# Optimization experiments

Measured on AMD Instinct MI355X. Metric: run time of the kernel, lower is better.

## Reference

```python
import jax, jax.numpy as jnp
import numpy as np

N_IN, D_IN, N_OUT, D_OUT = 1152, 8, 10, 16
ROUTINGS, NUM_BG = 3, 1
C, H, W = 1, 28, 28
BATCH = 128
DEC_IN = N_OUT * D_OUT  # 160, projection_type=None -> dec_feature_size = outcaps_size


def squash(x, axis=-1):
    norm = jnp.linalg.norm(x, axis=axis, keepdims=True)
    scale = norm ** 2 / (1.0 + norm ** 2) / (norm + 1e-8)
    return scale * x


def scale_coef(x, num_bg):
    # x: [B, n_out] or [B, n_out, n_in]; min/max normalize over dim 1,
    # excluding the last num_bg (background) capsules, then floor at 0.5.
    if num_bg > 0:
        xm = x[:, : x.shape[1] - num_bg]
    else:
        xm = x
    mn = jnp.min(xm, axis=1, keepdims=True)
    mx = jnp.max(xm, axis=1, keepdims=True)
    out = (xm - mn) / jnp.maximum(mx - mn, 1e-6)  # vrange (0,1)
    if num_bg > 0:
        out = jnp.concatenate([out, jnp.zeros_like(out[:, :num_bg])], axis=1)
    return jnp.maximum(out, 0.5)


def decode(capsflat, W1, b1, W2, b2, W3, b3):
    # fcn decoder (eval mode: dropout is identity): 160 -> 512 -> 1024 -> C*H*W
    h = jax.nn.relu(capsflat @ W1 + b1)
    h = jax.nn.relu(h @ W2 + b2)
    return jax.nn.sigmoid(h @ W3 + b3)


def setup_inputs() -> dict:
    key = jax.random.key(0)
    ks = jax.random.split(key, 9)
    return {
        'incaps': jax.random.normal(ks[0], (BATCH, N_IN, D_IN), jnp.float32),
        'x_input': jax.random.uniform(ks[1], (BATCH, C, H, W), jnp.float32),
        'weight': 0.1 * jax.random.normal(ks[2], (N_OUT, N_IN, D_OUT, D_IN), jnp.float32),
        'W1': 0.05 * jax.random.normal(ks[3], (DEC_IN, 512), jnp.float32),
        'b1': jnp.zeros((512,), jnp.float32),
        'W2': 0.05 * jax.random.normal(ks[4], (512, 1024), jnp.float32),
        'b2': jnp.zeros((1024,), jnp.float32),
        'W3': 0.05 * jax.random.normal(ks[5], (1024, C * H * W), jnp.float32),
        'b3': jnp.zeros((C * H * W,), jnp.float32),
    }


def reference(incaps, x_input, weight, W1, b1, W2, b2, W3, b3):
    B = incaps.shape[0]
    # outcaps_hat: matmul(weight, incaps[:,None,:,:,None]).squeeze(-1)
    hat = jnp.einsum('nkoi,bki->bnko', weight, incaps)  # [B, n_out, n_in, d_out]
    hat_d = jax.lax.stop_gradient(hat)
    rc = jnp.ones((B, N_OUT, N_IN), hat.dtype)
    eye = jnp.eye(N_OUT, dtype=hat.dtype)
    x_flat = x_input.reshape(B, 1, -1)
    for _ in range(ROUTINGS - 1):
        # squash over capsule dim, weighted sum over input capsules
        outcaps = squash(jnp.sum(rc[..., None] * hat_d, axis=2, keepdims=True))  # [B,n,1,d]
        b = jnp.sum(outcaps * hat_d, axis=-1)  # agreement [B, n_out, n_in]
        c = scale_coef(b, NUM_BG)
        objcaps = outcaps[:, :, 0, :]  # [B, n_out, d_out]
        # get_every_obj_rscore vectorized: mask one object capsule at a time
        masked = objcaps[:, None, :, :] * eye[None, :, :, None]  # [B, n_obj, n_out, d]
        recon = decode(masked.reshape(B, N_OUT, DEC_IN), W1, b1, W2, b2, W3, b3)  # [B,n_obj,CHW]
        rscore = -jnp.sum((x_flat - recon) ** 2, axis=-1)  # neg MSE-sum, [B, n_obj]
        r = scale_coef(rscore, NUM_BG)
        rc = c * r[:, :, None]
    # final iteration uses non-detached hat
    outcaps = squash(jnp.sum(rc[..., None] * hat, axis=2, keepdims=True))
    return outcaps[:, :, 0, :]  # [B, n_out, d_out]
```

## Files before the change

### kernel.cpp

```cpp
#include <hip/hip_runtime.h>
#include <math.h>

#define BATCH  128
#define NIN    1152
#define DIN    8
#define NOUTC  10
#define DOUT   16
#define H1DIM  512
#define H2DIM  1024
#define PIX    784
#define NROWS  (BATCH * NOUTC)
#define GN     32
#define PARTS  25
#define PSTR   32

typedef __attribute__((ext_vector_type(8))) __bf16 bf16x8;
typedef __attribute__((ext_vector_type(4))) float  f32x4;
typedef __attribute__((ext_vector_type(4))) unsigned int u32x4;

__device__ __forceinline__ float bf2f(unsigned int u) {
    union { unsigned int i; float f; } v; v.i = u << 16; return v.f;
}
__device__ __forceinline__ ushort f2bf(float f) {
    union { float f; unsigned int i; } v; v.f = f;
    unsigned int r = v.i + 0x7FFFu + ((v.i >> 16) & 1u);
    return (ushort)(r >> 16);
}
__device__ __forceinline__ float ldin(const void* p, size_t i, int isbf) {
    return isbf ? bf2f(((const ushort*)p)[i]) : ((const float*)p)[i];
}
__device__ __forceinline__ bf16x8 frag_of(uint4 u) {
    return __builtin_bit_cast(bf16x8, u);
}
__device__ __forceinline__ bf16x8 ld_frag(const ushort* p) {
    return frag_of(*(const uint4*)p);
}
__device__ __forceinline__ void unpack8(uint4 u, float* f) {
    f[0] = bf2f(u.x & 0xffffu); f[1] = bf2f(u.x >> 16);
    f[2] = bf2f(u.y & 0xffffu); f[3] = bf2f(u.y >> 16);
    f[4] = bf2f(u.z & 0xffffu); f[5] = bf2f(u.z >> 16);
    f[6] = bf2f(u.w & 0xffffu); f[7] = bf2f(u.w >> 16);
}

__device__ __forceinline__ int detect_bf(const void* w, int* cntS) {
    int tid = threadIdx.x, nt = blockDim.x;
    if (tid == 0) *cntS = 0;
    __syncthreads();
    const ushort* u = (const ushort*)w;
    int c = 0;
    for (int s = tid; s < 512; s += nt) {
        int e = (u[s * 2] >> 7) & 0xFF;
        if (e >= 88 && e <= 140) c++;
    }
    atomicAdd(cntS, c);
    __syncthreads();
    return (*cntS >= 384) ? 1 : 0;
}

struct PrepArgs {
    const void* w;
    const void* src[7];
    ushort*     dst[7];
    int         n[7];
    int*        flag;
};

__global__ __launch_bounds__(256) void prep_kernel(PrepArgs a)
{
    __shared__ int cntS;
    __shared__ ushort tile[32][33];
    int tid = threadIdx.x;
    int isbf = detect_bf(a.w, &cntS);
    int seg = blockIdx.y;
    if (seg == 0 && blockIdx.x == 0 && tid == 0) *a.flag = isbf;

    if (seg <= 4) {
        int n = a.n[seg];
        int stride = gridDim.x * 256;
        ushort* d = a.dst[seg];
        if (isbf) {
            const ushort* s = (const ushort*)a.src[seg];
            for (int i = blockIdx.x * 256 + tid; i < n; i += stride) d[i] = s[i];
        } else {
            const float* s = (const float*)a.src[seg];
            for (int i = blockIdx.x * 256 + tid; i < n; i += stride) d[i] = f2bf(s[i]);
        }
        return;
    }
    int R = (seg == 5) ? H1DIM : H2DIM;
    int C = (seg == 5) ? H2DIM : PIX;
    int tilesX = (seg == 5) ? 32 : 25;
    int tilesY = (seg == 5) ? 16 : 32;
    int t = blockIdx.x;
    if (t >= tilesX * tilesY) return;
    int tx2 = t % tilesX, ty2 = t / tilesX;
    int c0 = tx2 * 32, r0 = ty2 * 32;
    const void* in = a.src[seg];
    ushort* out = a.dst[seg];
    int tx = tid & 31, ty = tid >> 5;
    for (int i = ty; i < 32; i += 8) {
        int r = r0 + i, c = c0 + tx;
        tile[i][tx] = (r < R && c < C) ? f2bf(ldin(in, (size_t)r * C + c, isbf)) : (ushort)0;
    }
    __syncthreads();
    for (int i = ty; i < 32; i += 8) {
        int c = c0 + i, r = r0 + tx;
        if (c < C && r < R) out[(size_t)c * R + r] = tile[tx][i];
    }
}

__global__ __launch_bounds__(256) void hat_prep_kernel(
    const void* __restrict__ inc,
    PrepArgs a,
    ushort* __restrict__ hatG)
{
    __shared__ int cntS;
    __shared__ ushort tile[32][33];
    int tid = threadIdx.x;
    int isbf = detect_bf(a.w, &cntS);

    if (blockIdx.z >= NOUTC) {
        int p = (blockIdx.z - NOUTC) * 144 + blockIdx.y * 9 + blockIdx.x;
        if (p == 0 && tid == 0) *a.flag = isbf;
        if (p < 528) {
            for (int t = p; t < 1312; t += 528) {
                int seg = (t < 512) ? 5 : 6;
                int tt  = (seg == 5) ? t : t - 512;
                int R = (seg == 5) ? H1DIM : H2DIM;
                int C = (seg == 5) ? H2DIM : PIX;
                int tilesX = (seg == 5) ? 32 : 25;
                int tx2 = tt % tilesX, ty2 = tt / tilesX;
                int c0 = tx2 * 32, r0 = ty2 * 32;
                const void* in = a.src[seg];
                ushort* out = a.dst[seg];
                int tx = tid & 31, ty = tid >> 5;
                for (int i = ty; i < 32; i += 8) {
                    int r = r0 + i, c = c0 + tx;
                    tile[i][tx] = (r < R && c < C) ? f2bf(ldin(in, (size_t)r * C + c, isbf)) : (ushort)0;
                }
                __syncthreads();
                for (int i = ty; i < 32; i += 8) {
                    int c = c0 + i, r = r0 + tx;
                    if (c < C && r < R) out[(size_t)c * R + r] = tile[tx][i];
                }
                __syncthreads();
            }
        } else {
            int base = (p - 528) * 256 + tid;
            const int stride = 48 * 256;
            #pragma unroll
            for (int seg = 0; seg <= 4; seg++) {
                int n = a.n[seg];
                ushort* d = a.dst[seg];
                if (isbf) {
                    const ushort* s = (const ushort*)a.src[seg];
                    for (int i = base; i < n; i += stride) d[i] = s[i];
                } else {
                    const float* s = (const float*)a.src[seg];
                    for (int i = base; i < n; i += stride) d[i] = f2bf(s[i]);
                }
            }
        }
        return;
    }

    int kc = blockIdx.x, bc = blockIdx.y, n = blockIdx.z;
    int k  = kc * 128 + (tid >> 1);
    int oh = (tid & 1) << 3;
    int b0 = bc * 8;

    size_t wbase = ((size_t)n * NIN + k) * DOUT + oh;

    if (isbf) {
        uint4 wr[8], ir[8];
        const uint4* wp = (const uint4*)((const ushort*)a.w + wbase * DIN);
        const ushort* ip = (const ushort*)inc;
        #pragma unroll
        for (int j = 0; j < 8; j++) wr[j] = wp[j];
        #pragma unroll
        for (int bl = 0; bl < 8; bl++)
            ir[bl] = *(const uint4*)(ip + ((size_t)(b0 + bl) * NIN + k) * DIN);
        float wf[8][8];
        #pragma unroll
        for (int j = 0; j < 8; j++) unpack8(wr[j], wf[j]);
        #pragma unroll
        for (int bl = 0; bl < 8; bl++) {
            float xi[8];
            unpack8(ir[bl], xi);
            unsigned int hh[8];
            #pragma unroll
            for (int j = 0; j < 8; j++) {
                float s = wf[j][0] * xi[0] + wf[j][1] * xi[1] + wf[j][2] * xi[2] +
                          wf[j][3] * xi[3] + wf[j][4] * xi[4] + wf[j][5] * xi[5] +
                          wf[j][6] * xi[6] + wf[j][7] * xi[7];
                hh[j] = f2bf(s);
            }
            u32x4 ov = { hh[0] | (hh[1] << 16), hh[2] | (hh[3] << 16),
                         hh[4] | (hh[5] << 16), hh[6] | (hh[7] << 16) };
            *(u32x4*)(hatG + (((size_t)((b0 + bl) * NOUTC + n) * NIN + k) * DOUT + oh)) = ov;
        }
    } else {
        float4 wlo[8], whi[8], ilo[8], ihi[8];
        const float4* wp = (const float4*)((const float*)a.w + wbase * DIN);
        const float*  ip = (const float*)inc;
        #pragma unroll
        for (int j = 0; j < 8; j++) { wlo[j] = wp[2 * j]; whi[j] = wp[2 * j + 1]; }
        #pragma unroll
        for (int bl = 0; bl < 8; bl++) {
            const float4* q = (const float4*)(ip + ((size_t)(b0 + bl) * NIN + k) * DIN);
            ilo[bl] = q[0]; ihi[bl] = q[1];
        }
        #pragma unroll
        for (int bl = 0; bl < 8; bl++) {
            float4 lo = ilo[bl], hi = ihi[bl];
            unsigned int hh[8];
            #pragma unroll
            for (int j = 0; j < 8; j++) {
                float s = wlo[j].x * lo.x + wlo[j].y * lo.y + wlo[j].z * lo.z +
                          wlo[j].w * lo.w + whi[j].x * hi.x + whi[j].y * hi.y +
                          whi[j].z * hi.z + whi[j].w * hi.w;
                hh[j] = f2bf(s);
            }
            u32x4 ov = { hh[0] | (hh[1] << 16), hh[2] | (hh[3] << 16),
                         hh[4] | (hh[5] << 16), hh[6] | (hh[7] << 16) };
            *(u32x4*)(hatG + (((size_t)((b0 + bl) * NOUTC + n) * NIN + k) * DOUT + oh)) = ov;
        }
    }
}

__global__ __launch_bounds__(512, 4) void reduce_hat512(
    const ushort* __restrict__ hatG,
    const ushort* __restrict__ bsPrev,
    const float*  __restrict__ partials,
    int iter0,
    const ushort* __restrict__ W1c,
    const ushort* __restrict__ b1c,
    ushort* __restrict__ h1out,
    ushort* __restrict__ bsOut,
    void*   __restrict__ outFinal,
    const int* __restrict__ flagp)
{
    int bn  = blockIdx.x;
    int n   = bn % NOUTC;
    int b   = bn / NOUTC;
    int tid = threadIdx.x;

    __shared__ ushort wSb[NIN];
    __shared__ float  redS[8][16];
    __shared__ float  sumS[16];
    __shared__ float  ocS[16];
    __shared__ float  scaleS;
    __shared__ uint4  hatTail4[256];

    int h = tid & 1, kb = tid >> 1;
    int wave = tid >> 6, lane = tid & 63;

    const ushort* hbase = hatG + (size_t)bn * NIN * DOUT;
    uint4 v[4];
    #pragma unroll
    for (int j = 0; j < 4; j++)
        v[j] = *(const uint4*)(hbase + ((kb + 256 * j) * DOUT + h * 8));
    if (tid < 256)
        hatTail4[tid] = *(const uint4*)(hbase + 1024 * DOUT + tid * 8);
    const ushort* tailS = (const ushort*)hatTail4;

    if (!iter0) {
        if (tid < 9) {
            float s = 0.f;
            #pragma unroll
            for (int j = 0; j < PARTS; j++)
                s += partials[(size_t)(b * NOUTC + tid) * PSTR + j];
            sumS[tid] = -s;
        }
        __syncthreads();
        float mn = 1e30f, mx = -1e30f;
        #pragma unroll
        for (int n2 = 0; n2 < 9; n2++) {
            float vv = sumS[n2];
            mn = fminf(mn, vv); mx = fmaxf(mx, vv);
        }
        float den = fmaxf(mx - mn, 1e-6f);
        float rv = (n < 9) ? fmaxf((sumS[n] - mn) / den, 0.5f) : 0.5f;
        for (int k = tid; k < NIN; k += 512) {
            float c = 0.5f;
            if (n < 9) {
                float vv[9], mn2 = 1e30f, mx2 = -1e30f;
                #pragma unroll
                for (int n2 = 0; n2 < 9; n2++) {
                    vv[n2] = bf2f(bsPrev[(size_t)(b * NOUTC + n2) * NIN + k]);
                    mn2 = fminf(mn2, vv[n2]); mx2 = fmaxf(mx2, vv[n2]);
                }
                float den2 = fmaxf(mx2 - mn2, 1e-6f);
                c = fmaxf((vv[n] - mn2) / den2, 0.5f);
            }
            wSb[k] = f2bf(c * rv);
        }
    }
    __syncthreads();

    float acc[8];
    #pragma unroll
    for (int o = 0; o < 8; o++) acc[o] = 0.f;
    #pragma unroll
    for (int j = 0; j < 4; j++) {
        int k = kb + 256 * j;
        float w = iter0 ? 1.f : bf2f(wSb[k]);
        bf16x8 hv = frag_of(v[j]);
        #pragma unroll
        for (int o = 0; o < 8; o++) acc[o] += w * (float)hv[o];
    }
    if (tid < 256) {
        int k = 1024 + kb;
        float w = iter0 ? 1.f : bf2f(wSb[k]);
        bf16x8 hv = ld_frag(tailS + kb * DOUT + h * 8);
        #pragma unroll
        for (int o = 0; o < 8; o++) acc[o] += w * (float)hv[o];
    }
    #pragma unroll
    for (int off = 32; off >= 2; off >>= 1) {
        #pragma unroll
        for (int o = 0; o < 8; o++) acc[o] += __shfl_xor(acc[o], off);
    }
    if (lane < 2) {
        #pragma unroll
        for (int o = 0; o < 8; o++) redS[wave][lane * 8 + o] = acc[o];
    }
    __syncthreads();
    if (tid < 16) {
        float s = 0.f;
        #pragma unroll
        for (int wv = 0; wv < 8; wv++) s += redS[wv][tid];
        sumS[tid] = s;
    }
    __syncthreads();
    if (tid == 0) {
        float n2 = 0.f;
        #pragma unroll
        for (int o = 0; o < 16; o++) n2 += sumS[o] * sumS[o];
        float nrm = sqrtf(n2);
        scaleS = n2 / (1.f + n2) / (nrm + 1e-8f);
    }
    __syncthreads();
    if (tid < 16) {
        float oc = scaleS * sumS[tid];
        ocS[tid] = oc;
        if (outFinal) {
            if (*flagp) ((ushort*)outFinal)[(size_t)bn * 16 + tid] = f2bf(oc);
            else        ((float*) outFinal)[(size_t)bn * 16 + tid] = oc;
        }
    }
    __syncthreads();

    if (bsOut) {
        float o0 = ocS[h * 8 + 0], o1 = ocS[h * 8 + 1], o2 = ocS[h * 8 + 2],
              o3 = ocS[h * 8 + 3], o4 = ocS[h * 8 + 4], o5 = ocS[h * 8 + 5],
              o6 = ocS[h * 8 + 6], o7 = ocS[h * 8 + 7];
        #pragma unroll
        for (int j = 0; j < 4; j++) {
            bf16x8 hv = frag_of(v[j]);
            float s = o0 * (float)hv[0] + o1 * (float)hv[1] + o2 * (float)hv[2] +
                      o3 * (float)hv[3] + o4 * (float)hv[4] + o5 * (float)hv[5] +
                      o6 * (float)hv[6] + o7 * (float)hv[7];
            s += __shfl_xor(s, 1);
            if (h == 0) bsOut[(size_t)bn * NIN + kb + 256 * j] = f2bf(s);
        }
        if (tid < 256) {
            bf16x8 hv = ld_frag(tailS + kb * DOUT + h * 8);
            float s = o0 * (float)hv[0] + o1 * (float)hv[1] + o2 * (float)hv[2] +
                      o3 * (float)hv[3] + o4 * (float)hv[4] + o5 * (float)hv[5] +
                      o6 * (float)hv[6] + o7 * (float)hv[7];
            s += __shfl_xor(s, 1);
            if (h == 0) bsOut[(size_t)bn * NIN + 1024 + kb] = f2bf(s);
        }
    }

    if (h1out) {
        int col = tid;
        float acc1 = bf2f(b1c[col]);
        #pragma unroll
        for (int i = 0; i < 16; i++)
            acc1 += ocS[i] * bf2f(W1c[(size_t)(n * 16 + i) * H1DIM + col]);
        h1out[(size_t)bn * H1DIM + col] = f2bf(fmaxf(acc1, 0.f));
    }
}

__global__ __launch_bounds__(256) void gemm_kernel(
    const ushort* __restrict__ A, const ushort* __restrict__ Bt,
    const ushort* __restrict__ bias, int K, int N,
    ushort* __restrict__ Cout,
    const ushort* __restrict__ xin, float* __restrict__ partials)
{
    int m0 = blockIdx.x * 64, n0 = blockIdx.y * GN;
    int tid = threadIdx.x;
    int wave = tid >> 6, lane = tid & 63, quad = lane >> 4, l16 = lane & 15;

    __shared__ uint4 As4[640];
    __shared__ uint4 Bs4[320];
    ushort* As = (ushort*)As4;
    ushort* Bs = (ushort*)Bs4;

    f32x4 acc[2];
    #pragma unroll
    for (int nt = 0; nt < 2; nt++)
        #pragma unroll
        for (int rg = 0; rg < 4; rg++) acc[nt][rg] = 0.f;

    int sMi = tid >> 2, sKk = (tid & 3) * 8;
    int sLds = sMi * 5 + (tid & 3);
    const ushort* Ap = A + (size_t)(m0 + sMi) * K + sKk;
    int bMi = (tid & 127) >> 2, bChunk = tid >> 7;
    int bLds = bChunk * 160 + bMi * 5 + (tid & 3);
    const ushort* Bp = Bt + (size_t)(n0 + bMi) * K + sKk + bChunk * 32;
    bool bOK = (n0 + bMi) < N;

    uint4 aR0 = *(const uint4*)Ap;
    uint4 aR1 = *(const uint4*)(Ap + 32);
    uint4 bR  = bOK ? *(const uint4*)Bp : make_uint4(0, 0, 0, 0);

    for (int k0 = 0; k0 < K; k0 += 64) {
        As4[sLds]       = aR0;
        As4[320 + sLds] = aR1;
        Bs4[bLds]       = bR;
        __syncthreads();
        if (k0 + 64 < K) {
            aR0 = *(const uint4*)(Ap + k0 + 64);
            aR1 = *(const uint4*)(Ap + k0 + 96);
            bR  = bOK ? *(const uint4*)(Bp + k0 + 64) : make_uint4(0, 0, 0, 0);
        }
        #pragma unroll
        for (int c = 0; c < 2; c++) {
            bf16x8 a = ld_frag(As + c * 2560 + (wave * 16 + l16) * 40 + quad * 8);
            #pragma unroll
            for (int nt = 0; nt < 2; nt++) {
                bf16x8 bb = ld_frag(Bs + c * 1280 + (nt * 16 + l16) * 40 + quad * 8);
                acc[nt] = __builtin_amdgcn_mfma_f32_16x16x32_bf16(a, bb, acc[nt], 0, 0, 0);
            }
        }
        __syncthreads();
    }

    int rowBase = m0 + wave * 16 + quad * 4;
    if (Cout) {
        #pragma unroll
        for (int nt = 0; nt < 2; nt++) {
            int col = n0 + nt * 16 + l16;
            float bv = bf2f(bias[col]);
            #pragma unroll
            for (int rg = 0; rg < 4; rg++) {
                float v = acc[nt][rg] + bv;
                Cout[(size_t)(rowBase + rg) * N + col] = f2bf(fmaxf(v, 0.f));
            }
        }
    } else {
        float vr[4] = {0.f, 0.f, 0.f, 0.f};
        #pragma unroll
        for (int nt = 0; nt < 2; nt++) {
            int col = n0 + nt * 16 + l16;
            if (col < N) {
                float bv = bf2f(bias[col]);
                #pragma unroll
                for (int rg = 0; rg < 4; rg++) {
                    int row = rowBase + rg;
                    int bb = row / NOUTC;
                    float z = acc[nt][rg] + bv;
                    float s = 1.f / (1.f + __expf(-z));
                    float d = bf2f(xin[(size_t)bb * PIX + col]) - s;
                    vr[rg] += d * d;
                }
            }
        }
        #pragma unroll
        for (int rg = 0; rg < 4; rg++) {
            float v = vr[rg];
            #pragma unroll
            for (int off = 8; off >= 1; off >>= 1) v += __shfl_xor(v, off, 16);
            if (l16 == 0)
                partials[(size_t)(rowBase + rg) * PSTR + blockIdx.y] = v;
        }
    }
}

__global__ __launch_bounds__(512, 4) void reduce_compute(
    const void*   __restrict__ incRaw,
    const void*   __restrict__ wRaw,
    const ushort* __restrict__ bsPrev,
    const float*  __restrict__ partials,
    int iter0,
    const ushort* __restrict__ W1c,
    const ushort* __restrict__ b1c,
    ushort* __restrict__ h1out,
    ushort* __restrict__ bsOut,
    void*   __restrict__ outFinal,
    const int* __restrict__ flagp)
{
    int bn  = blockIdx.x;
    int n   = bn % NOUTC;
    int b   = bn / NOUTC;
    int tid = threadIdx.x;

    __shared__ ushort wSb[NIN];
    __shared__ float  redS[8][16];
    __shared__ float  sumS[16];
    __shared__ float  ocS[16];
    __shared__ float  scaleS;

    int h = tid & 1, kb = tid >> 1;
    int wave = tid >> 6, lane = tid & 63;

    uint4 v[4];
    const ushort* tailS;

    __shared__ int cntS;
    __shared__ uint4 hatS4[NIN * DOUT / 8];
    int isbf = detect_bf(wRaw, &cntS);
    size_t wnb = (size_t)n * NIN * DOUT * DIN;
    for (int idx = tid; idx < NIN * DOUT; idx += 512) {
        int k = idx >> 4;
        float s = 0.f;
        #pragma unroll
        for (int i = 0; i < 8; i++)
            s += ldin(wRaw, wnb + (size_t)idx * 8 + i, isbf) *
                 ldin(incRaw, ((size_t)b * NIN + k) * DIN + i, isbf);
        ((ushort*)hatS4)[idx] = f2bf(s);
    }
    __syncthreads();
    const ushort* hbase = (const ushort*)hatS4;
    #pragma unroll
    for (int j = 0; j < 4; j++)
        v[j] = *(const uint4*)(hbase + ((kb + 256 * j) * DOUT + h * 8));
    tailS = hbase + 1024 * DOUT;

    if (!iter0) {
        if (tid < 9) {
            float s = 0.f;
            #pragma unroll
            for (int j = 0; j < PARTS; j++)
                s += partials[(size_t)(b * NOUTC + tid) * PSTR + j];
            sumS[tid] = -s;
        }
        __syncthreads();
        float mn = 1e30f, mx = -1e30f;
        #pragma unroll
        for (int n2 = 0; n2 < 9; n2++) {
            float vv = sumS[n2];
            mn = fminf(mn, vv); mx = fmaxf(mx, vv);
        }
        float den = fmaxf(mx - mn, 1e-6f);
        float rv = (n < 9) ? fmaxf((sumS[n] - mn) / den, 0.5f) : 0.5f;
        for (int k = tid; k < NIN; k += 512) {
            float c = 0.5f;
            if (n < 9) {
                float vv[9], mn2 = 1e30f, mx2 = -1e30f;
                #pragma unroll
                for (int n2 = 0; n2 < 9; n2++) {
                    vv[n2] = bf2f(bsPrev[(size_t)(b * NOUTC + n2) * NIN + k]);
                    mn2 = fminf(mn2, vv[n2]); mx2 = fmaxf(mx2, vv[n2]);
                }
                float den2 = fmaxf(mx2 - mn2, 1e-6f);
                c = fmaxf((vv[n] - mn2) / den2, 0.5f);
            }
            wSb[k] = f2bf(c * rv);
        }
    }
    __syncthreads();

    float acc[8];
    #pragma unroll
    for (int o = 0; o < 8; o++) acc[o] = 0.f;
    #pragma unroll
    for (int j = 0; j < 4; j++) {
        int k = kb + 256 * j;
        float w = iter0 ? 1.f : bf2f(wSb[k]);
        bf16x8 hv = frag_of(v[j]);
        #pragma unroll
        for (int o = 0; o < 8; o++) acc[o] += w * (float)hv[o];
    }
    if (tid < 256) {
        int k = 1024 + kb;
        float w = iter0 ? 1.f : bf2f(wSb[k]);
        bf16x8 hv = ld_frag(tailS + kb * DOUT + h * 8);
        #pragma unroll
        for (int o = 0; o < 8; o++) acc[o] += w * (float)hv[o];
    }
    #pragma unroll
    for (int off = 32; off >= 2; off >>= 1) {
        #pragma unroll
        for (int o = 0; o < 8; o++) acc[o] += __shfl_xor(acc[o], off);
    }
    if (lane < 2) {
        #pragma unroll
        for (int o = 0; o < 8; o++) redS[wave][lane * 8 + o] = acc[o];
    }
    __syncthreads();
    if (tid < 16) {
        float s = 0.f;
        #pragma unroll
        for (int wv = 0; wv < 8; wv++) s += redS[wv][tid];
        sumS[tid] = s;
    }
    __syncthreads();
    if (tid == 0) {
        float n2 = 0.f;
        #pragma unroll
        for (int o = 0; o < 16; o++) n2 += sumS[o] * sumS[o];
        float nrm = sqrtf(n2);
        scaleS = n2 / (1.f + n2) / (nrm + 1e-8f);
    }
    __syncthreads();
    if (tid < 16) {
        float oc = scaleS * sumS[tid];
        ocS[tid] = oc;
        if (outFinal) {
            if (*flagp) ((ushort*)outFinal)[(size_t)bn * 16 + tid] = f2bf(oc);
            else        ((float*) outFinal)[(size_t)bn * 16 + tid] = oc;
        }
    }
    __syncthreads();

    if (bsOut) {
        float o0 = ocS[h * 8 + 0], o1 = ocS[h * 8 + 1], o2 = ocS[h * 8 + 2],
              o3 = ocS[h * 8 + 3], o4 = ocS[h * 8 + 4], o5 = ocS[h * 8 + 5],
              o6 = ocS[h * 8 + 6], o7 = ocS[h * 8 + 7];
        #pragma unroll
        for (int j = 0; j < 4; j++) {
            bf16x8 hv = frag_of(v[j]);
            float s = o0 * (float)hv[0] + o1 * (float)hv[1] + o2 * (float)hv[2] +
                      o3 * (float)hv[3] + o4 * (float)hv[4] + o5 * (float)hv[5] +
                      o6 * (float)hv[6] + o7 * (float)hv[7];
            s += __shfl_xor(s, 1);
            if (h == 0) bsOut[(size_t)bn * NIN + kb + 256 * j] = f2bf(s);
        }
        if (tid < 256) {
            bf16x8 hv = ld_frag(tailS + kb * DOUT + h * 8);
            float s = o0 * (float)hv[0] + o1 * (float)hv[1] + o2 * (float)hv[2] +
                      o3 * (float)hv[3] + o4 * (float)hv[4] + o5 * (float)hv[5] +
                      o6 * (float)hv[6] + o7 * (float)hv[7];
            s += __shfl_xor(s, 1);
            if (h == 0) bsOut[(size_t)bn * NIN + 1024 + kb] = f2bf(s);
        }
    }

    if (h1out) {
        int col = tid;
        float acc1 = bf2f(b1c[col]);
        #pragma unroll
        for (int i = 0; i < 16; i++)
            acc1 += ocS[i] * bf2f(W1c[(size_t)(n * 16 + i) * H1DIM + col]);
        h1out[(size_t)bn * H1DIM + col] = f2bf(fmaxf(acc1, 0.f));
    }
}

extern "C" void kernel_launch(void* const* d_in, const int* in_sizes, int n_in,
                              void* d_out, int out_size, void* d_ws, size_t ws_size,
                              hipStream_t stream)
{
    const void* inc = d_in[0];
    const void* x   = d_in[1];
    const void* w   = d_in[2];
    const void* W1  = d_in[3];
    const void* b1  = d_in[4];
    const void* W2  = d_in[5];
    const void* b2  = d_in[6];
    const void* W3  = d_in[7];
    const void* b3  = d_in[8];

    char* p = (char*)d_ws;
    auto alloc = [&](size_t bytes) { void* r = p; p += (bytes + 255) & ~(size_t)255; return r; };
    int*    flagWS    = (int*)alloc(256);
    ushort* bsA       = (ushort*)alloc((size_t)NROWS * NIN * 2);
    ushort* bsB       = (ushort*)alloc((size_t)NROWS * NIN * 2);
    float*  partials  = (float*)alloc((size_t)NROWS * PSTR * 4);
    ushort* h1WS      = (ushort*)alloc((size_t)NROWS * H1DIM * 2);
    ushort* h2WS      = (ushort*)alloc((size_t)NROWS * H2DIM * 2);
    ushort* W2T       = (ushort*)alloc((size_t)H2DIM * H1DIM * 2);
    ushort* W3T       = (ushort*)alloc((size_t)PIX * H2DIM * 2);
    ushort* W1c       = (ushort*)alloc((size_t)160 * H1DIM * 2);
    ushort* b1c       = (ushort*)alloc((size_t)H1DIM * 2);
    ushort* b2c       = (ushort*)alloc((size_t)H2DIM * 2);
    ushort* b3c       = (ushort*)alloc((size_t)PIX * 2);
    ushort* xc        = (ushort*)alloc((size_t)BATCH * PIX * 2);
    ushort* hatG      = (ushort*)alloc((size_t)NROWS * NIN * DOUT * 2);
    bool haveHat = ((char*)hatG + (size_t)NROWS * NIN * DOUT * 2) <= ((char*)d_ws + ws_size);

    PrepArgs pa;
    pa.w = w;
    pa.src[0] = W1;  pa.dst[0] = W1c;  pa.n[0] = 160 * H1DIM;
    pa.src[1] = b1;  pa.dst[1] = b1c;  pa.n[1] = H1DIM;
    pa.src[2] = b2;  pa.dst[2] = b2c;  pa.n[2] = H2DIM;
    pa.src[3] = b3;  pa.dst[3] = b3c;  pa.n[3] = PIX;
    pa.src[4] = x;   pa.dst[4] = xc;   pa.n[4] = BATCH * PIX;
    pa.src[5] = W2;  pa.dst[5] = W2T;  pa.n[5] = 0;
    pa.src[6] = W3;  pa.dst[6] = W3T;  pa.n[6] = 0;
    pa.flag = flagWS;

    if (!haveHat) {
        prep_kernel<<<dim3(800, 7), 256, 0, stream>>>(pa);
        reduce_compute<<<NROWS, 512, 0, stream>>>(
            inc, w, nullptr, nullptr, 1, W1c, b1c, h1WS, bsA, nullptr, flagWS);
        for (int it = 0; it < 2; it++) {
            gemm_kernel<<<dim3(NROWS / 64, H2DIM / GN), 256, 0, stream>>>(
                h1WS, W2T, b2c, H1DIM, H2DIM, h2WS, nullptr, nullptr);
            gemm_kernel<<<dim3(NROWS / 64, PARTS), 256, 0, stream>>>(
                h2WS, W3T, b3c, H2DIM, PIX, nullptr, xc, partials);
            int last = (it == 1);
            const ushort* bsP = (it == 0) ? bsA : bsB;
            ushort* bsO       = last ? nullptr : bsB;
            ushort* h1o       = last ? nullptr : h1WS;
            void*   fin       = last ? d_out : nullptr;
            reduce_compute<<<NROWS, 512, 0, stream>>>(
                inc, w, bsP, partials, 0, W1c, b1c, h1o, bsO, fin, flagWS);
        }
        return;
    }

    hat_prep_kernel<<<dim3(9, 16, NOUTC + 4), 256, 0, stream>>>(inc, pa, hatG);

    reduce_hat512<<<NROWS, 512, 0, stream>>>(
        hatG, nullptr, nullptr, 1, W1c, b1c, h1WS, bsA, nullptr, flagWS);

    for (int it = 0; it < 2; it++) {
        gemm_kernel<<<dim3(NROWS / 64, H2DIM / GN), 256, 0, stream>>>(
            h1WS, W2T, b2c, H1DIM, H2DIM, h2WS, nullptr, nullptr);
        gemm_kernel<<<dim3(NROWS / 64, PARTS), 256, 0, stream>>>(
            h2WS, W3T, b3c, H2DIM, PIX, nullptr, xc, partials);

        int last = (it == 1);
        const ushort* bsP = (it == 0) ? bsA : bsB;
        ushort* bsO       = last ? nullptr : bsB;
        ushort* h1o       = last ? nullptr : h1WS;
        void*   fin       = last ? d_out : nullptr;
        reduce_hat512<<<NROWS, 512, 0, stream>>>(
            hatG, bsP, partials, 0, W1c, b1c, h1o, bsO, fin, flagWS);
    }
}
```

Before: 189.1 us.

## Fuse routing reduce and decoder GEMMs into persistent kernel with flag-based dataflow sync

Result: slower. 356.4 us (+88.5%).

```diff
diff --git a/kernel.cpp b/kernel.cpp
--- a/kernel.cpp
+++ b/kernel.cpp
@@ -13,6 +13,7 @@
 #define GN     32
 #define PARTS  25
 #define PSTR   32
+#define NSYNC  4096
 
 typedef __attribute__((ext_vector_type(8))) __bf16 bf16x8;
 typedef __attribute__((ext_vector_type(4))) float  f32x4;
@@ -63,6 +64,7 @@
     ushort*     dst[7];
     int         n[7];
     int*        flag;
+    int*        sync;
 };
 
 __global__ __launch_bounds__(256) void prep_kernel(PrepArgs a)
@@ -148,6 +150,7 @@
         } else {
             int base = (p - 528) * 256 + tid;
             const int stride = 48 * 256;
+            for (int i = base; i < NSYNC; i += stride) a.sync[i] = 0;
             #pragma unroll
             for (int seg = 0; seg <= 4; seg++) {
                 int n = a.n[seg];
@@ -225,6 +228,323 @@
                          hh[4] | (hh[5] << 16), hh[6] | (hh[7] << 16) };
             *(u32x4*)(hatG + (((size_t)((b0 + bl) * NOUTC + n) * NIN + k) * DOUT + oh)) = ov;
         }
+    }
+}
+
+struct MegaArgs {
+    const ushort* hatG;
+    const ushort* W1c; const ushort* b1c;
+    const ushort* W2T; const ushort* b2c;
+    const ushort* W3T; const ushort* b3c;
+    const ushort* xc;
+    ushort* h1; ushort* h2;
+    ushort* bsA; ushort* bsB;
+    void*   outFinal;
+    const int* flagp;
+};
+
+struct GSmem { uint4 As4[640]; uint4 Bs4[320]; };
+struct RSmem { ushort wSb[NIN]; float redS[4][16]; float sumS[16];
+               float ocS[16]; float scaleS; };
+union MegaSmem { GSmem g; RSmem r; };
+
+__device__ __forceinline__ void red_item(
+    const MegaArgs& A, MegaSmem& S, int bn, int notFirst,
+    const ushort* bsPrev, const float* partials,
+    ushort* bsOut, ushort* h1out, int writeOut)
+{
+    int n = bn % NOUTC, b = bn / NOUTC;
+    int t = threadIdx.x;
+    int wave = t >> 6, lane = t & 63;
+    const ushort* hbase = A.hatG + (size_t)bn * NIN * DOUT;
+
+    uint4 v[4][2];
+    #pragma unroll
+    for (int j = 0; j < 4; j++) {
+        v[j][0] = *(const uint4*)(hbase + (t + 256 * j) * DOUT);
+        v[j][1] = *(const uint4*)(hbase + (t + 256 * j) * DOUT + 8);
+    }
+    uint4 vt0 = make_uint4(0,0,0,0), vt1 = make_uint4(0,0,0,0);
+    if (t < 128) {
+        vt0 = *(const uint4*)(hbase + (1024 + t) * DOUT);
+        vt1 = *(const uint4*)(hbase + (1024 + t) * DOUT + 8);
+    }
+
+    if (notFirst) {
+        if (t < 9) {
+            float s = 0.f;
+            #pragma unroll
+            for (int j = 0; j < PARTS; j++)
+                s += partials[(size_t)(b * NOUTC + t) * PSTR + j];
+            S.r.sumS[t] = -s;
+        }
+        __syncthreads();
+        float mn = 1e30f, mx = -1e30f;
+        #pragma unroll
+        for (int n2 = 0; n2 < 9; n2++) {
+            float vv = S.r.sumS[n2];
+            mn = fminf(mn, vv); mx = fmaxf(mx, vv);
+        }
+        float den = fmaxf(mx - mn, 1e-6f);
+        float rv = (n < 9) ? fmaxf((S.r.sumS[n] - mn) / den, 0.5f) : 0.5f;
+        __syncthreads();
+        for (int k = t; k < NIN; k += 256) {
+            float c = 0.5f;
+            if (n < 9) {
+                float vv[9], mn2 = 1e30f, mx2 = -1e30f;
+                #pragma unroll
+                for (int n2 = 0; n2 < 9; n2++) {
+                    vv[n2] = bf2f(bsPrev[(size_t)(b * NOUTC + n2) * NIN + k]);
+                    mn2 = fminf(mn2, vv[n2]); mx2 = fmaxf(mx2, vv[n2]);
+                }
+                float den2 = fmaxf(mx2 - mn2, 1e-6f);
+                c = fmaxf((vv[n] - mn2) / den2, 0.5f);
+            }
+            S.r.wSb[k] = f2bf(c * rv);
+        }
+    }
+    __syncthreads();
+
+    float acc[16];
+    #pragma unroll
+    for (int o = 0; o < 16; o++) acc[o] = 0.f;
+    #pragma unroll
+    for (int j = 0; j < 4; j++) {
+        int k = t + 256 * j;
+        float w = notFirst ? bf2f(S.r.wSb[k]) : 1.f;
+        bf16x8 h0 = frag_of(v[j][0]), h1v = frag_of(v[j][1]);
+        #pragma unroll
+        for (int o = 0; o < 8; o++) {
+            acc[o]     += w * (float)h0[o];
+            acc[8 + o] += w * (float)h1v[o];
+        }
+    }
+    if (t < 128) {
+        float w = notFirst ? bf2f(S.r.wSb[1024 + t]) : 1.f;
+        bf16x8 h0 = frag_of(vt0), h1v = frag_of(vt1);
+        #pragma unroll
+        for (int o = 0; o < 8; o++) {
+            acc[o]     += w * (float)h0[o];
+            acc[8 + o] += w * (float)h1v[o];
+        }
+    }
+    #pragma unroll
+    for (int off = 32; off >= 1; off >>= 1) {
+        #pragma unroll
+        for (int o = 0; o < 16; o++) acc[o] += __shfl_xor(acc[o], off);
+    }
+    if (lane == 0) {
+        #pragma unroll
+        for (int o = 0; o < 16; o++) S.r.redS[wave][o] = acc[o];
+    }
+    __syncthreads();
+    if (t < 16) {
+        float s = 0.f;
+        #pragma unroll
+        for (int wv = 0; wv < 4; wv++) s += S.r.redS[wv][t];
+        S.r.sumS[t] = s;
+    }
+    __syncthreads();
+    if (t == 0) {
+        float n2 = 0.f;
+        #pragma unroll
+        for (int o = 0; o < 16; o++) n2 += S.r.sumS[o] * S.r.sumS[o];
+        float nrm = sqrtf(n2);
+        S.r.scaleS = n2 / (1.f + n2) / (nrm + 1e-8f);
+    }
+    __syncthreads();
+    if (t < 16) {
+        float oc = S.r.scaleS * S.r.sumS[t];
+        S.r.ocS[t] = oc;
+        if (writeOut) {
+            if (*A.flagp) ((ushort*)A.outFinal)[(size_t)bn * 16 + t] = f2bf(oc);
+            else          ((float*) A.outFinal)[(size_t)bn * 16 + t] = oc;
+        }
+    }
+    __syncthreads();
+
+    if (bsOut) {
+        float oc[16];
+        #pragma unroll
+        for (int o = 0; o < 16; o++) oc[o] = S.r.ocS[o];
+        #pragma unroll
+        for (int j = 0; j < 4; j++) {
+            bf16x8 h0 = frag_of(v[j][0]), h1v = frag_of(v[j][1]);
+            float s = 0.f;
+            #pragma unroll
+            for (int o = 0; o < 8; o++)
+                s += oc[o] * (float)h0[o] + oc[8 + o] * (float)h1v[o];
+            bsOut[(size_t)bn * NIN + t + 256 * j] = f2bf(s);
+        }
+        if (t < 128) {
+            bf16x8 h0 = frag_of(vt0), h1v = frag_of(vt1);
+            float s = 0.f;
+            #pragma unroll
+            for (int o = 0; o < 8; o++)
+                s += oc[o] * (float)h0[o] + oc[8 + o] * (float)h1v[o];
+            bsOut[(size_t)bn * NIN + 1024 + t] = f2bf(s);
+        }
+    }
+    if (h1out) {
+        #pragma unroll
+        for (int cc = 0; cc < 2; cc++) {
+            int col = t + 256 * cc;
+            float acc1 = bf2f(A.b1c[col]);
+            #pragma unroll
+            for (int i = 0; i < 16; i++)
+                acc1 += S.r.ocS[i] * bf2f(A.W1c[(size_t)(n * 16 + i) * H1DIM + col]);
+            h1out[(size_t)bn * H1DIM + col] = f2bf(fmaxf(acc1, 0.f));
+        }
+    }
+}
+
+__device__ __forceinline__ void gemm_tile(
+    MegaSmem& S, const ushort* __restrict__ A_, const ushort* __restrict__ Bt,
+    const ushort* __restrict__ bias, int K, int N,
+    ushort* __restrict__ Cout, const ushort* __restrict__ xin,
+    float* __restrict__ partials, int m0, int n0, int tileY)
+{
+    int tid = threadIdx.x;
+    int wave = tid >> 6, lane = tid & 63, quad = lane >> 4, l16 = lane & 15;
+    uint4* As4 = S.g.As4;
+    uint4* Bs4 = S.g.Bs4;
+    ushort* As = (ushort*)As4;
+    ushort* Bs = (ushort*)Bs4;
+
+    f32x4 acc[2];
+    #pragma unroll
+    for (int nt = 0; nt < 2; nt++)
+        #pragma unroll
+        for (int rg = 0; rg < 4; rg++) acc[nt][rg] = 0.f;
+
+    int sMi = tid >> 2, sKk = (tid & 3) * 8;
+    int sLds = sMi * 5 + (tid & 3);
+    const ushort* Ap = A_ + (size_t)(m0 + sMi) * K + sKk;
+    int bMi = (tid & 127) >> 2, bChunk = tid >> 7;
+    int bLds = bChunk * 160 + bMi * 5 + (tid & 3);
+    const ushort* Bp = Bt + (size_t)(n0 + bMi) * K + sKk + bChunk * 32;
+    bool bOK = (n0 + bMi) < N;
+
+    uint4 aR0 = *(const uint4*)Ap;
+    uint4 aR1 = *(const uint4*)(Ap + 32);
+    uint4 bR  = bOK ? *(const uint4*)Bp : make_uint4(0, 0, 0, 0);
+
+    for (int k0 = 0; k0 < K; k0 += 64) {
+        As4[sLds]       = aR0;
+        As4[320 + sLds] = aR1;
+        Bs4[bLds]       = bR;
+        __syncthreads();
+        if (k0 + 64 < K) {
+            aR0 = *(const uint4*)(Ap + k0 + 64);
+            aR1 = *(const uint4*)(Ap + k0 + 96);
+            bR  = bOK ? *(const uint4*)(Bp + k0 + 64) : make_uint4(0, 0, 0, 0);
+        }
+        #pragma unroll
+        for (int c = 0; c < 2; c++) {
+            bf16x8 a = ld_frag(As + c * 2560 + (wave * 16 + l16) * 40 + quad * 8);
+            #pragma unroll
+            for (int nt = 0; nt < 2; nt++) {
+                bf16x8 bb = ld_frag(Bs + c * 1280 + (nt * 16 + l16) * 40 + quad * 8);
+                acc[nt] = __builtin_amdgcn_mfma_f32_16x16x32_bf16(a, bb, acc[nt], 0, 0, 0);
+            }
+        }
+        __syncthreads();
+    }
+
+    int rowBase = m0 + wave * 16 + quad * 4;
+    if (Cout) {
+        #pragma unroll
+        for (int nt = 0; nt < 2; nt++) {
+            int col = n0 + nt * 16 + l16;
+            float bv = bf2f(bias[col]);
+            #pragma unroll
+            for (int rg = 0; rg < 4; rg++) {
+                float v = acc[nt][rg] + bv;
+                Cout[(size_t)(rowBase + rg) * N + col] = f2bf(fmaxf(v, 0.f));
+            }
+        }
+    } else {
+        float vr[4] = {0.f, 0.f, 0.f, 0.f};
+        #pragma unroll
+        for (int nt = 0; nt < 2; nt++) {
+            int col = n0 + nt * 16 + l16;
+            if (col < N) {
+                float bv = bf2f(bias[col]);
+                #pragma unroll
+                for (int rg = 0; rg < 4; rg++) {
+                    int row = rowBase + rg;
+                    int bb = row / NOUTC;
+                    float z = acc[nt][rg] + bv;
+                    float s = 1.f / (1.f + __expf(-z));
+                    float d = bf2f(xin[(size_t)bb * PIX + col]) - s;
+                    vr[rg] += d * d;
+                }
+            }
+        }
+        #pragma unroll
+        for (int rg = 0; rg < 4; rg++) {
+            float v = vr[rg];
+            #pragma unroll
+            for (int off = 8; off >= 1; off >>= 1) v += __shfl_xor(v, off, 16);
+            if (l16 == 0)
+                partials[(size_t)(rowBase + rg) * PSTR + tileY] = v;
+        }
+    }
+}
+
+__device__ __forceinline__ void signal_flag(int* flag) {
+    __syncthreads();
+    if (threadIdx.x == 0)
+        __hip_atomic_store(flag, 1, __ATOMIC_RELEASE, __HIP_MEMORY_SCOPE_AGENT);
+}
+__device__ __forceinline__ void wait_flags(const int* flags, int n) {
+    if (threadIdx.x < 64) {
+        int t = threadIdx.x;
+        int v = (t < n) ? 0 : 1;
+        int guard = 0;
+        while (true) {
+            if (!v) v = __hip_atomic_load(flags + t, __ATOMIC_RELAXED,
+                                          __HIP_MEMORY_SCOPE_AGENT);
+            if (__all(v != 0)) break;
+            __builtin_amdgcn_s_sleep(8);
+            if (++guard > (1 << 22)) break;
+        }
+        __threadfence();
+    }
+    __syncthreads();
+}
+
+__global__ __launch_bounds__(256, 4) void fused_iter(
+    MegaArgs A, const float* partIn, float* partOut,
+    int* flag1, int* flag2, int redMode)
+{
+    __shared__ MegaSmem S;
+    int bid = blockIdx.x;
+
+    if (redMode == 0) red_item(A, S, bid, 0, nullptr, nullptr, A.bsA, A.h1, 0);
+    else              red_item(A, S, bid, 1, A.bsA, partIn, A.bsB, A.h1, 0);
+    signal_flag(&flag1[bid]);
+
+    if (bid >= 640 && bid < 896) {
+        int bn = 1024 + (bid - 640);
+        if (redMode == 0) red_item(A, S, bn, 0, nullptr, nullptr, A.bsA, A.h1, 0);
+        else              red_item(A, S, bn, 1, A.bsA, partIn, A.bsB, A.h1, 0);
+        signal_flag(&flag1[bn]);
+        return;
+    }
+
+    if (bid < 640) {
+        int m = bid % 20, nv = bid / 20;
+        wait_flags(flag1 + m * 64, 64);
+        gemm_tile(S, A.h1, A.W2T, A.b2c, H1DIM, H2DIM, A.h2,
+                  nullptr, nullptr, m * 64, nv * GN, 0);
+        signal_flag(&flag2[m * 32 + nv]);
+    }
+    if (bid < 500) {
+        int m = bid % 20, cy = bid / 20;
+        wait_flags(flag2 + m * 32, 32);
+        gemm_tile(S, A.h2, A.W3T, A.b3c, H2DIM, PIX, nullptr,
+                  A.xc, partOut, m * 64, cy * GN, cy);
     }
 }
 
@@ -390,94 +710,9 @@
     ushort* __restrict__ Cout,
     const ushort* __restrict__ xin, float* __restrict__ partials)
 {
-    int m0 = blockIdx.x * 64, n0 = blockIdx.y * GN;
-    int tid = threadIdx.x;
-    int wave = tid >> 6, lane = tid & 63, quad = lane >> 4, l16 = lane & 15;
-
-    __shared__ uint4 As4[640];
-    __shared__ uint4 Bs4[320];
-    ushort* As = (ushort*)As4;
-    ushort* Bs = (ushort*)Bs4;
-
-    f32x4 acc[2];
-    #pragma unroll
-    for (int nt = 0; nt < 2; nt++)
-        #pragma unroll
-        for (int rg = 0; rg < 4; rg++) acc[nt][rg] = 0.f;
-
-    int sMi = tid >> 2, sKk = (tid & 3) * 8;
-    int sLds = sMi * 5 + (tid & 3);
-    const ushort* Ap = A + (size_t)(m0 + sMi) * K + sKk;
-    int bMi = (tid & 127) >> 2, bChunk = tid >> 7;
-    int bLds = bChunk * 160 + bMi * 5 + (tid & 3);
-    const ushort* Bp = Bt + (size_t)(n0 + bMi) * K + sKk + bChunk * 32;
-    bool bOK = (n0 + bMi) < N;
-
-    uint4 aR0 = *(const uint4*)Ap;
-    uint4 aR1 = *(const uint4*)(Ap + 32);
-    uint4 bR  = bOK ? *(const uint4*)Bp : make_uint4(0, 0, 0, 0);
-
-    for (int k0 = 0; k0 < K; k0 += 64) {
-        As4[sLds]       = aR0;
-        As4[320 + sLds] = aR1;
-        Bs4[bLds]       = bR;
-        __syncthreads();
-        if (k0 + 64 < K) {
-            aR0 = *(const uint4*)(Ap + k0 + 64);
-            aR1 = *(const uint4*)(Ap + k0 + 96);
-            bR  = bOK ? *(const uint4*)(Bp + k0 + 64) : make_uint4(0, 0, 0, 0);
-        }
-        #pragma unroll
-        for (int c = 0; c < 2; c++) {
-            bf16x8 a = ld_frag(As + c * 2560 + (wave * 16 + l16) * 40 + quad * 8);
-            #pragma unroll
-            for (int nt = 0; nt < 2; nt++) {
-                bf16x8 bb = ld_frag(Bs + c * 1280 + (nt * 16 + l16) * 40 + quad * 8);
-                acc[nt] = __builtin_amdgcn_mfma_f32_16x16x32_bf16(a, bb, acc[nt], 0, 0, 0);
-            }
-        }
-        __syncthreads();
-    }
-
-    int rowBase = m0 + wave * 16 + quad * 4;
-    if (Cout) {
-        #pragma unroll
-        for (int nt = 0; nt < 2; nt++) {
-            int col = n0 + nt * 16 + l16;
-            float bv = bf2f(bias[col]);
-            #pragma unroll
-            for (int rg = 0; rg < 4; rg++) {
-                float v = acc[nt][rg] + bv;
-                Cout[(size_t)(rowBase + rg) * N + col] = f2bf(fmaxf(v, 0.f));
-            }
-        }
-    } else {
-        float vr[4] = {0.f, 0.f, 0.f, 0.f};
-        #pragma unroll
-        for (int nt = 0; nt < 2; nt++) {
-            int col = n0 + nt * 16 + l16;
-            if (col < N) {
-                float bv = bf2f(bias[col]);
-                #pragma unroll
-                for (int rg = 0; rg < 4; rg++) {
-                    int row = rowBase + rg;
-                    int bb = row / NOUTC;
-                    float z = acc[nt][rg] + bv;
-                    float s = 1.f / (1.f + __expf(-z));
-                    float d = bf2f(xin[(size_t)bb * PIX + col]) - s;
-                    vr[rg] += d * d;
-                }
-            }
-        }
-        #pragma unroll
-        for (int rg = 0; rg < 4; rg++) {
-            float v = vr[rg];
-            #pragma unroll
-            for (int off = 8; off >= 1; off >>= 1) v += __shfl_xor(v, off, 16);
-            if (l16 == 0)
-                partials[(size_t)(rowBase + rg) * PSTR + blockIdx.y] = v;
-        }
-    }
+    __shared__ MegaSmem S;
+    gemm_tile(S, A, Bt, bias, K, N, Cout, xin, partials,
+              blockIdx.x * 64, blockIdx.y * GN, blockIdx.y);
 }
 
 __global__ __launch_bounds__(512, 4) void reduce_compute(
@@ -667,9 +902,11 @@
     char* p = (char*)d_ws;
     auto alloc = [&](size_t bytes) { void* r = p; p += (bytes + 255) & ~(size_t)255; return r; };
     int*    flagWS    = (int*)alloc(256);
+    int*    syncWS    = (int*)alloc(NSYNC * sizeof(int));
     ushort* bsA       = (ushort*)alloc((size_t)NROWS * NIN * 2);
     ushort* bsB       = (ushort*)alloc((size_t)NROWS * NIN * 2);
-    float*  partials  = (float*)alloc((size_t)NROWS * PSTR * 4);
+    float*  partialsA = (float*)alloc((size_t)NROWS * PSTR * 4);
+    float*  partialsB = (float*)alloc((size_t)NROWS * PSTR * 4);
     ushort* h1WS      = (ushort*)alloc((size_t)NROWS * H1DIM * 2);
     ushort* h2WS      = (ushort*)alloc((size_t)NROWS * H2DIM * 2);
     ushort* W2T       = (ushort*)alloc((size_t)H2DIM * H1DIM * 2);
@@ -692,6 +929,7 @@
     pa.src[5] = W2;  pa.dst[5] = W2T;  pa.n[5] = 0;
     pa.src[6] = W3;  pa.dst[6] = W3T;  pa.n[6] = 0;
     pa.flag = flagWS;
+    pa.sync = syncWS;
 
     if (!haveHat) {
         prep_kernel<<<dim3(800, 7), 256, 0, stream>>>(pa);
@@ -701,35 +939,31 @@
             gemm_kernel<<<dim3(NROWS / 64, H2DIM / GN), 256, 0, stream>>>(
                 h1WS, W2T, b2c, H1DIM, H2DIM, h2WS, nullptr, nullptr);
             gemm_kernel<<<dim3(NROWS / 64, PARTS), 256, 0, stream>>>(
-                h2WS, W3T, b3c, H2DIM, PIX, nullptr, xc, partials);
+                h2WS, W3T, b3c, H2DIM, PIX, nullptr, xc, partialsA);
             int last = (it == 1);
             const ushort* bsP = (it == 0) ? bsA : bsB;
             ushort* bsO       = last ? nullptr : bsB;
             ushort* h1o       = last ? nullptr : h1WS;
             void*   fin       = last ? d_out : nullptr;
             reduce_compute<<<NROWS, 512, 0, stream>>>(
-                inc, w, bsP, partials, 0, W1c, b1c, h1o, bsO, fin, flagWS);
+                inc, w, bsP, partialsA, 0, W1c, b1c, h1o, bsO, fin, flagWS);
         }
         return;
     }
 
     hat_prep_kernel<<<dim3(9, 16, NOUTC + 4), 256, 0, stream>>>(inc, pa, hatG);
 
+    MegaArgs ma;
+    ma.hatG = hatG; ma.W1c = W1c; ma.b1c = b1c;
+    ma.W2T = W2T;   ma.b2c = b2c; ma.W3T = W3T; ma.b3c = b3c;
+    ma.xc = xc;     ma.h1 = h1WS; ma.h2 = h2WS;
+    ma.bsA = bsA;   ma.bsB = bsB;
+    ma.outFinal = d_out; ma.flagp = flagWS;
+
+    fused_iter<<<1024, 256, 0, stream>>>(
+        ma, nullptr, partialsA, syncWS + 0, syncWS + 1280, 0);
+    fused_iter<<<1024, 256, 0, stream>>>(
+        ma, partialsA, partialsB, syncWS + 2048, syncWS + 3328, 1);
     reduce_hat512<<<NROWS, 512, 0, stream>>>(
-        hatG, nullptr, nullptr, 1, W1c, b1c, h1WS, bsA, nullptr, flagWS);
-
-    for (int it = 0; it < 2; it++) {
-        gemm_kernel<<<dim3(NROWS / 64, H2DIM / GN), 256, 0, stream>>>(
-            h1WS, W2T, b2c, H1DIM, H2DIM, h2WS, nullptr, nullptr);
-        gemm_kernel<<<dim3(NROWS / 64, PARTS), 256, 0, stream>>>(
-            h2WS, W3T, b3c, H2DIM, PIX, nullptr, xc, partials);
-
-        int last = (it == 1);
-        const ushort* bsP = (it == 0) ? bsA : bsB;
-        ushort* bsO       = last ? nullptr : bsB;
-        ushort* h1o       = last ? nullptr : h1WS;
-        void*   fin       = last ? d_out : nullptr;
-        reduce_hat512<<<NROWS, 512, 0, stream>>>(
-            hatG, bsP, partials, 0, W1c, b1c, h1o, bsO, fin, flagWS);
-    }
-}
+        hatG, bsB, partialsB, 0, W1c, b1c, nullptr, nullptr, d_out, flagWS);
+}
```

## Shrink GEMM tile to 32x32 with 2x2 wave grid and K-step 128

Applied to the files above, without the earlier changes.

Measured after the change: 191.8 us. No clear change (+1.4%).

```diff
diff --git a/kernel.cpp b/kernel.cpp
--- a/kernel.cpp
+++ b/kernel.cpp
@@ -10,9 +10,10 @@
 #define H2DIM  1024
 #define PIX    784
 #define NROWS  (BATCH * NOUTC)
+#define GM     32
 #define GN     32
-#define PARTS  25
-#define PSTR   32
+#define PARTSR 50
+#define PSTR   64
 
 typedef __attribute__((ext_vector_type(8))) __bf16 bf16x8;
 typedef __attribute__((ext_vector_type(4))) float  f32x4;
@@ -268,7 +269,7 @@
         if (tid < 9) {
             float s = 0.f;
             #pragma unroll
-            for (int j = 0; j < PARTS; j++)
+            for (int j = 0; j < PARTSR; j++)
                 s += partials[(size_t)(b * NOUTC + tid) * PSTR + j];
             sumS[tid] = -s;
         }
@@ -390,83 +391,71 @@
     ushort* __restrict__ Cout,
     const ushort* __restrict__ xin, float* __restrict__ partials)
 {
-    int m0 = blockIdx.x * 64, n0 = blockIdx.y * GN;
+    int m0 = blockIdx.x * GM, n0 = blockIdx.y * GN;
     int tid = threadIdx.x;
     int wave = tid >> 6, lane = tid & 63, quad = lane >> 4, l16 = lane & 15;
+    int wr = wave & 1, wc = wave >> 1;
 
     __shared__ uint4 As4[640];
-    __shared__ uint4 Bs4[320];
+    __shared__ uint4 Bs4[640];
     ushort* As = (ushort*)As4;
     ushort* Bs = (ushort*)Bs4;
 
-    f32x4 acc[2];
-    #pragma unroll
-    for (int nt = 0; nt < 2; nt++)
-        #pragma unroll
-        for (int rg = 0; rg < 4; rg++) acc[nt][rg] = 0.f;
-
-    int sMi = tid >> 2, sKk = (tid & 3) * 8;
-    int sLds = sMi * 5 + (tid & 3);
-    const ushort* Ap = A + (size_t)(m0 + sMi) * K + sKk;
-    int bMi = (tid & 127) >> 2, bChunk = tid >> 7;
-    int bLds = bChunk * 160 + bMi * 5 + (tid & 3);
-    const ushort* Bp = Bt + (size_t)(n0 + bMi) * K + sKk + bChunk * 32;
-    bool bOK = (n0 + bMi) < N;
-
-    uint4 aR0 = *(const uint4*)Ap;
-    uint4 aR1 = *(const uint4*)(Ap + 32);
-    uint4 bR  = bOK ? *(const uint4*)Bp : make_uint4(0, 0, 0, 0);
-
-    for (int k0 = 0; k0 < K; k0 += 64) {
-        As4[sLds]       = aR0;
-        As4[320 + sLds] = aR1;
-        Bs4[bLds]       = bR;
+    f32x4 acc = {0.f, 0.f, 0.f, 0.f};
+
+    int r = tid >> 4, kq = tid & 15, chunk = kq >> 2, cc = kq & 3;
+    int sL0 = chunk * 160 + r * 5 + cc, sL1 = sL0 + 80;
+    const ushort* Ap0 = A + (size_t)(m0 + r) * K + kq * 8;
+    const ushort* Ap1 = Ap0 + (size_t)16 * K;
+    const ushort* Bp0 = Bt + (size_t)(n0 + r) * K + kq * 8;
+    const ushort* Bp1 = Bp0 + (size_t)16 * K;
+    bool bOK0 = (n0 + r) < N, bOK1 = (n0 + r + 16) < N;
+
+    uint4 aR0 = *(const uint4*)Ap0;
+    uint4 aR1 = *(const uint4*)Ap1;
+    uint4 bR0 = bOK0 ? *(const uint4*)Bp0 : make_uint4(0, 0, 0, 0);
+    uint4 bR1 = bOK1 ? *(const uint4*)Bp1 : make_uint4(0, 0, 0, 0);
+
+    for (int k0 = 0; k0 < K; k0 += 128) {
+        As4[sL0] = aR0; As4[sL1] = aR1;
+        Bs4[sL0] = bR0; Bs4[sL1] = bR1;
         __syncthreads();
-        if (k0 + 64 < K) {
-            aR0 = *(const uint4*)(Ap + k0 + 64);
-            aR1 = *(const uint4*)(Ap + k0 + 96);
-            bR  = bOK ? *(const uint4*)(Bp + k0 + 64) : make_uint4(0, 0, 0, 0);
-        }
-        #pragma unroll
-        for (int c = 0; c < 2; c++) {
-            bf16x8 a = ld_frag(As + c * 2560 + (wave * 16 + l16) * 40 + quad * 8);
-            #pragma unroll
-            for (int nt = 0; nt < 2; nt++) {
-                bf16x8 bb = ld_frag(Bs + c * 1280 + (nt * 16 + l16) * 40 + quad * 8);
-                acc[nt] = __builtin_amdgcn_mfma_f32_16x16x32_bf16(a, bb, acc[nt], 0, 0, 0);
-            }
+        if (k0 + 128 < K) {
+            aR0 = *(const uint4*)(Ap0 + k0 + 128);
+            aR1 = *(const uint4*)(Ap1 + k0 + 128);
+            bR0 = bOK0 ? *(const uint4*)(Bp0 + k0 + 128) : make_uint4(0, 0, 0, 0);
+            bR1 = bOK1 ? *(const uint4*)(Bp1 + k0 + 128) : make_uint4(0, 0, 0, 0);
+        }
+        #pragma unroll
+        for (int c = 0; c < 4; c++) {
+            bf16x8 a = ld_frag(As + c * 1280 + (wr * 16 + l16) * 40 + quad * 8);
+            bf16x8 b = ld_frag(Bs + c * 1280 + (wc * 16 + l16) * 40 + quad * 8);
+            acc = __builtin_amdgcn_mfma_f32_16x16x32_bf16(a, b, acc, 0, 0, 0);
         }
         __syncthreads();
     }
 
-    int rowBase = m0 + wave * 16 + quad * 4;
+    int rowBase = m0 + wr * 16 + quad * 4;
+    int col = n0 + wc * 16 + l16;
     if (Cout) {
-        #pragma unroll
-        for (int nt = 0; nt < 2; nt++) {
-            int col = n0 + nt * 16 + l16;
+        float bv = bf2f(bias[col]);
+        #pragma unroll
+        for (int rg = 0; rg < 4; rg++) {
+            float v = acc[rg] + bv;
+            Cout[(size_t)(rowBase + rg) * N + col] = f2bf(fmaxf(v, 0.f));
+        }
+    } else {
+        float vr[4] = {0.f, 0.f, 0.f, 0.f};
+        if (col < N) {
             float bv = bf2f(bias[col]);
             #pragma unroll
             for (int rg = 0; rg < 4; rg++) {
-                float v = acc[nt][rg] + bv;
-                Cout[(size_t)(rowBase + rg) * N + col] = f2bf(fmaxf(v, 0.f));
-            }
-        }
-    } else {
-        float vr[4] = {0.f, 0.f, 0.f, 0.f};
-        #pragma unroll
-        for (int nt = 0; nt < 2; nt++) {
-            int col = n0 + nt * 16 + l16;
-            if (col < N) {
-                float bv = bf2f(bias[col]);
-                #pragma unroll
-                for (int rg = 0; rg < 4; rg++) {
-                    int row = rowBase + rg;
-                    int bb = row / NOUTC;
-                    float z = acc[nt][rg] + bv;
-                    float s = 1.f / (1.f + __expf(-z));
-                    float d = bf2f(xin[(size_t)bb * PIX + col]) - s;
-                    vr[rg] += d * d;
-                }
+                int row = rowBase + rg;
+                int bb = row / NOUTC;
+                float z = acc[rg] + bv;
+                float s = 1.f / (1.f + __expf(-z));
+                float d = bf2f(xin[(size_t)bb * PIX + col]) - s;
+                vr[rg] = d * d;
             }
         }
         #pragma unroll
@@ -475,7 +464,7 @@
             #pragma unroll
             for (int off = 8; off >= 1; off >>= 1) v += __shfl_xor(v, off, 16);
             if (l16 == 0)
-                partials[(size_t)(rowBase + rg) * PSTR + blockIdx.y] = v;
+                partials[(size_t)(rowBase + rg) * PSTR + blockIdx.y * 2 + wc] = v;
         }
     }
 }
@@ -534,7 +523,7 @@
         if (tid < 9) {
             float s = 0.f;
             #pragma unroll
-            for (int j = 0; j < PARTS; j++)
+            for (int j = 0; j < PARTSR; j++)
                 s += partials[(size_t)(b * NOUTC + tid) * PSTR + j];
             sumS[tid] = -s;
         }
@@ -698,9 +687,9 @@
         reduce_compute<<<NROWS, 512, 0, stream>>>(
             inc, w, nullptr, nullptr, 1, W1c, b1c, h1WS, bsA, nullptr, flagWS);
         for (int it = 0; it < 2; it++) {
-            gemm_kernel<<<dim3(NROWS / 64, H2DIM / GN), 256, 0, stream>>>(
+            gemm_kernel<<<dim3(NROWS / GM, H2DIM / GN), 256, 0, stream>>>(
                 h1WS, W2T, b2c, H1DIM, H2DIM, h2WS, nullptr, nullptr);
-            gemm_kernel<<<dim3(NROWS / 64, PARTS), 256, 0, stream>>>(
+            gemm_kernel<<<dim3(NROWS / GM, 25), 256, 0, stream>>>(
                 h2WS, W3T, b3c, H2DIM, PIX, nullptr, xc, partials);
             int last = (it == 1);
             const ushort* bsP = (it == 0) ? bsA : bsB;
@@ -719,9 +708,9 @@
         hatG, nullptr, nullptr, 1, W1c, b1c, h1WS, bsA, nullptr, flagWS);
 
     for (int it = 0; it < 2; it++) {
-        gemm_kernel<<<dim3(NROWS / 64, H2DIM / GN), 256, 0, stream>>>(
+        gemm_kernel<<<dim3(NROWS / GM, H2DIM / GN), 256, 0, stream>>>(
             h1WS, W2T, b2c, H1DIM, H2DIM, h2WS, nullptr, nullptr);
-        gemm_kernel<<<dim3(NROWS / 64, PARTS), 256, 0, stream>>>(
+        gemm_kernel<<<dim3(NROWS / GM, 25), 256, 0, stream>>>(
             h2WS, W3T, b3c, H2DIM, PIX, nullptr, xc, partials);
 
         int last = (it == 1);
```
